# Kernel optimization log

Hardware: AMD Instinct MI355X
Metric: run time of the kernel (lower is better)

## Reference

```python
import jax, jax.numpy as jnp
import numpy as np

N = 100000
E = 1200000


def _gcn_norm(edge_index, num_nodes):
    # Add self-loops and compute symmetric normalization (PyG GCNConv default).
    row = jnp.concatenate([edge_index[0], jnp.arange(num_nodes, dtype=edge_index.dtype)])
    col = jnp.concatenate([edge_index[1], jnp.arange(num_nodes, dtype=edge_index.dtype)])
    deg = jax.ops.segment_sum(jnp.ones_like(col, dtype=jnp.float32), col, num_segments=num_nodes)
    dinv = jnp.where(deg > 0, jax.lax.rsqrt(jnp.maximum(deg, 1.0)), 0.0)
    norm = dinv[row] * dinv[col]  # [E+N]
    return row, col, norm


def _gcn_conv(x, W, b, row, col, norm, num_nodes):
    h = x @ W                      # [N, out] dense transform first (fewer bytes to gather)
    msg = h[row] * norm[:, None]   # gather + edge-wise scale
    out = jax.ops.segment_sum(msg, col, num_segments=num_nodes)  # scatter-add to targets
    return out + b


def setup_inputs() -> dict:
    key = jax.random.key(0)
    k1, k2, k3, k4 = jax.random.split(key, 4)
    x = jax.random.normal(k1, (N, 128), dtype=jnp.float32)
    edge_index = jax.random.randint(k2, (2, E), 0, N, dtype=jnp.int64)
    W1 = jax.random.normal(k3, (128, 256), dtype=jnp.float32) * (1.0 / np.sqrt(128))
    b1 = jnp.zeros((256,), dtype=jnp.float32)
    W2 = jax.random.normal(k4, (256, 40), dtype=jnp.float32) * (1.0 / np.sqrt(256))
    b2 = jnp.zeros((40,), dtype=jnp.float32)
    return {"x": x, "edge_index": edge_index, "W1": W1, "b1": b1, "W2": W2, "b2": b2}


def reference(x, edge_index, W1, b1, W2, b2):
    row, col, norm = _gcn_norm(edge_index, N)
    h = _gcn_conv(x, W1, b1, row, col, norm, N)
    h = jax.nn.relu(h)
    # dropout omitted: eval mode (training=False) is identity
    return _gcn_conv(h, W2, b2, row, col, norm, N)
```

## Files before the change

### kernel.cpp

```cpp
#include <hip/hip_runtime.h>
#include <hip/hip_bf16.h>

#define NN 100000
#define EE 1200000
#define F1 128
#define F2 256
#define F3 40
#define MROWS 64
#define NBUK ((NN + 255) / 256)
#define NBLK 256
#define CHUNK ((EE + NBLK - 1) / NBLK)
#define DCAP 4096
#define XB ((NN * 64 + 255) / 256)

typedef __bf16 bf16x8 __attribute__((ext_vector_type(8)));
typedef float  f32x4  __attribute__((ext_vector_type(4)));

__device__ __forceinline__ unsigned short f2bf(float f) {
    unsigned u = __float_as_uint(f);
    return (unsigned short)((u + 0x7fffu + ((u >> 16) & 1u)) >> 16);
}
__device__ __forceinline__ float bflo(unsigned v) { return __uint_as_float(v << 16); }
__device__ __forceinline__ float bfhi(unsigned v) { return __uint_as_float(v & 0xffff0000u); }

__global__ __launch_bounds__(256) void k_hist(const int* __restrict__ col,
                                              int* __restrict__ hist) {
    __shared__ int lh[NBUK];
    for (int i = threadIdx.x; i < NBUK; i += 256) lh[i] = 0;
    __syncthreads();
    int e0 = blockIdx.x * CHUNK;
    int e1 = min(e0 + CHUNK, EE);
    for (int e = e0 + threadIdx.x; e < e1; e += 256) {
        int c = col[e];
        if ((unsigned)c < (unsigned)NN) atomicAdd(&lh[c >> 8], 1);
    }
    __syncthreads();
    for (int i = threadIdx.x; i < NBUK; i += 256) hist[i * NBLK + blockIdx.x] = lh[i];
}

__global__ __launch_bounds__(256) void k_scanbin(int* __restrict__ hist,
                                                 int* __restrict__ bintot) {
    __shared__ int s[NBLK];
    int b = blockIdx.x;
    int v = hist[b * NBLK + threadIdx.x];
    s[threadIdx.x] = v;
    __syncthreads();
    int acc = v;
    for (int d = 1; d < NBLK; d <<= 1) {
        int add = (threadIdx.x >= d) ? s[threadIdx.x - d] : 0;
        __syncthreads();
        acc += add;
        s[threadIdx.x] = acc;
        __syncthreads();
    }
    hist[b * NBLK + threadIdx.x] = acc - v;
    if (threadIdx.x == NBLK - 1) bintot[b] = acc;
}

__global__ __launch_bounds__(512) void k_scanbase(const int* __restrict__ bintot,
                                                  int* __restrict__ binbase) {
    __shared__ int s[512];
    int v = (threadIdx.x < NBUK) ? bintot[threadIdx.x] : 0;
    s[threadIdx.x] = v;
    __syncthreads();
    int acc = v;
    for (int d = 1; d < 512; d <<= 1) {
        int add = (threadIdx.x >= d) ? s[threadIdx.x - d] : 0;
        __syncthreads();
        acc += add;
        s[threadIdx.x] = acc;
        __syncthreads();
    }
    if (threadIdx.x < NBUK) binbase[threadIdx.x] = acc - v;
    if (threadIdx.x == NBUK - 1) binbase[NBUK] = acc;
}

__global__ __launch_bounds__(256) void k_scat(const int* __restrict__ row,
                                              const int* __restrict__ col,
                                              const int* __restrict__ hist,
                                              const int* __restrict__ binbase,
                                              unsigned* __restrict__ rec) {
    __shared__ int lcur[NBUK];
    for (int i = threadIdx.x; i < NBUK; i += 256)
        lcur[i] = binbase[i] + hist[i * NBLK + blockIdx.x];
    __syncthreads();
    int e0 = blockIdx.x * CHUNK;
    int e1 = min(e0 + CHUNK, EE);
    for (int e = e0 + threadIdx.x; e < e1; e += 256) {
        int r = row[e], c = col[e];
        if ((unsigned)c < (unsigned)NN) {
            int pos = atomicAdd(&lcur[c >> 8], 1);
            rec[pos] = ((unsigned)r & 0xFFFFFFu) | ((unsigned)(c & 255) << 24);
        }
    }
}

__global__ __launch_bounds__(256) void k_csr(const int* __restrict__ binbase,
                                             const unsigned* __restrict__ rec,
                                             int* __restrict__ eidx,
                                             int* __restrict__ cnt,
                                             int* __restrict__ cursor,
                                             float* __restrict__ dinv) {
    __shared__ int lcnt[256];
    __shared__ int s[256];
    __shared__ int lcur[256];
    __shared__ int lde[DCAP];
    const int b = blockIdx.x;
    const int tid = threadIdx.x;
    lcnt[tid] = 0;
    __syncthreads();
    const int base = binbase[b];
    const int nb = min(binbase[b + 1] - base, DCAP);
    for (int j = tid; j < nb; j += 256) atomicAdd(&lcnt[rec[base + j] >> 24], 1);
    __syncthreads();
    int cv = lcnt[tid];
    s[tid] = cv;
    __syncthreads();
    int acc = cv;
    for (int d = 1; d < 256; d <<= 1) {
        int add = (tid >= d) ? s[tid - d] : 0;
        __syncthreads();
        acc += add;
        s[tid] = acc;
        __syncthreads();
    }
    int excl = acc - cv;
    lcur[tid] = excl;
    const int node = (b << 8) + tid;
    if (node < NN) {
        cnt[node] = cv;
        cursor[node] = base + excl + cv;
        dinv[node] = rsqrtf((float)(cv + 1));
    }
    __syncthreads();
    for (int j = tid; j < nb; j += 256) {
        unsigned v = rec[base + j];
        int pos = atomicAdd(&lcur[v >> 24], 1);
        lde[pos] = (int)(v & 0xFFFFFFu);
    }
    __syncthreads();
    for (int j = tid; j < nb; j += 256) eidx[base + j] = lde[j];
}

__global__ void k_prep(const float2* __restrict__ x, const float* __restrict__ dinv,
                       unsigned* __restrict__ xh,
                       const float* __restrict__ W1, const float* __restrict__ W2,
                       __hip_bfloat16* __restrict__ W1p, __hip_bfloat16* __restrict__ W2p) {
    if (blockIdx.x < XB) {
        int idx = blockIdx.x * 256 + threadIdx.x;
        if (idx < NN * 64) {
            float d = dinv[idx >> 6];
            float2 v = x[idx];
            xh[idx] = (unsigned)f2bf(v.x * d) | ((unsigned)f2bf(v.y * d) << 16);
        }
    } else {
        int idx = (blockIdx.x - XB) * 256 + threadIdx.x;
        if (idx < F1 * F2) {
            int k = idx / F2, col = idx - (idx / F2) * F2;
            int k8 = k >> 3, j = k & 7;
            W1p[((size_t)(k8 * F2 + col) << 3) + j] = __float2bfloat16(W1[(size_t)k * F2 + col]);
        } else if (idx < F1 * F2 + F2 * 48) {
            int i2 = idx - F1 * F2;
            int k = i2 / 48, col = i2 - (i2 / 48) * 48;
            int k8 = k >> 3, j = k & 7;
            float v = (col < F3) ? W2[(size_t)k * F3 + col] : 0.0f;
            W2p[((size_t)(k8 * 48 + col) << 3) + j] = __float2bfloat16(v);
        }
    }
}

__global__ __launch_bounds__(256) void k_agg1(const int* __restrict__ cursor,
                                              const int* __restrict__ cnt,
                                              const int* __restrict__ eidx,
                                              const float* __restrict__ dinv,
                                              const unsigned* __restrict__ xh,
                                              unsigned* __restrict__ agg) {
    int node = blockIdx.x * 4 + (threadIdx.x >> 6);
    int lane = threadIdx.x & 63;
    if (node >= NN) return;
    unsigned vs = xh[((size_t)node << 6) + lane];
    float a0 = bflo(vs), a1 = bfhi(vs);
    int n = cnt[node];
    int s = cursor[node] - n;
    int k = 0;
    for (; k + 7 < n; k += 8) {
        int r0 = eidx[s + k + 0], r1 = eidx[s + k + 1];
        int r2 = eidx[s + k + 2], r3 = eidx[s + k + 3];
        int r4 = eidx[s + k + 4], r5 = eidx[s + k + 5];
        int r6 = eidx[s + k + 6], r7 = eidx[s + k + 7];
        unsigned v0 = xh[((size_t)r0 << 6) + lane];
        unsigned v1 = xh[((size_t)r1 << 6) + lane];
        unsigned v2 = xh[((size_t)r2 << 6) + lane];
        unsigned v3 = xh[((size_t)r3 << 6) + lane];
        unsigned v4 = xh[((size_t)r4 << 6) + lane];
        unsigned v5 = xh[((size_t)r5 << 6) + lane];
        unsigned v6 = xh[((size_t)r6 << 6) + lane];
        unsigned v7 = xh[((size_t)r7 << 6) + lane];
        a0 += bflo(v0); a1 += bfhi(v0);
        a0 += bflo(v1); a1 += bfhi(v1);
        a0 += bflo(v2); a1 += bfhi(v2);
        a0 += bflo(v3); a1 += bfhi(v3);
        a0 += bflo(v4); a1 += bfhi(v4);
        a0 += bflo(v5); a1 += bfhi(v5);
        a0 += bflo(v6); a1 += bfhi(v6);
        a0 += bflo(v7); a1 += bfhi(v7);
    }
    for (; k + 3 < n; k += 4) {
        int r0 = eidx[s + k + 0], r1 = eidx[s + k + 1];
        int r2 = eidx[s + k + 2], r3 = eidx[s + k + 3];
        unsigned v0 = xh[((size_t)r0 << 6) + lane];
        unsigned v1 = xh[((size_t)r1 << 6) + lane];
        unsigned v2 = xh[((size_t)r2 << 6) + lane];
        unsigned v3 = xh[((size_t)r3 << 6) + lane];
        a0 += bflo(v0); a1 += bfhi(v0);
        a0 += bflo(v1); a1 += bfhi(v1);
        a0 += bflo(v2); a1 += bfhi(v2);
        a0 += bflo(v3); a1 += bfhi(v3);
    }
    for (; k < n; ++k) {
        unsigned v0 = xh[((size_t)eidx[s + k] << 6) + lane];
        a0 += bflo(v0); a1 += bfhi(v0);
    }
    float d = dinv[node];
    agg[((size_t)node << 6) + lane] = (unsigned)f2bf(a0 * d) | ((unsigned)f2bf(a1 * d) << 16);
}

__global__ __launch_bounds__(256) void k_gemm_mfma(
    const __hip_bfloat16* __restrict__ agg, const __hip_bfloat16* __restrict__ W1p,
    const float* __restrict__ b1, const __hip_bfloat16* __restrict__ W2p,
    const float* __restrict__ dinv, unsigned short* __restrict__ tg) {
    __shared__ __hip_bfloat16 h_s[MROWS][F2 + 8];
    const int i0   = blockIdx.x * MROWS;
    const int wave = threadIdx.x >> 6;
    const int lane = threadIdx.x & 63;
    const int m = lane & 15, q = lane >> 4;
    const int rowA = i0 + wave * 16 + m;

    f32x4 acc[16];
#pragma unroll
    for (int c = 0; c < 16; ++c) acc[c] = (f32x4){0.f, 0.f, 0.f, 0.f};

#pragma unroll
    for (int s = 0; s < 4; ++s) {
        bf16x8 a;
#pragma unroll
        for (int j = 0; j < 8; ++j) a[j] = (__bf16)0.0f;
        if (rowA < NN) a = *(const bf16x8*)(agg + (size_t)rowA * F1 + s * 32 + q * 8);
        const __hip_bfloat16* bp = W1p + ((size_t)(4 * s + q) * F2) * 8;
#pragma unroll
        for (int c = 0; c < 16; ++c) {
            bf16x8 b = *(const bf16x8*)(bp + ((size_t)(c * 16 + m) << 3));
            acc[c] = __builtin_amdgcn_mfma_f32_16x16x32_bf16(a, b, acc[c], 0, 0, 0);
        }
    }

#pragma unroll
    for (int c = 0; c < 16; ++c) {
        int col = c * 16 + m;
        float bj = b1[col];
#pragma unroll
        for (int r = 0; r < 4; ++r) {
            int lr = wave * 16 + q * 4 + r;
            h_s[lr][col] = __float2bfloat16(fmaxf(acc[c][r] + bj, 0.0f));
        }
    }
    __syncthreads();

    f32x4 acc2[3];
#pragma unroll
    for (int c = 0; c < 3; ++c) acc2[c] = (f32x4){0.f, 0.f, 0.f, 0.f};

#pragma unroll
    for (int s = 0; s < 8; ++s) {
        bf16x8 a = *(const bf16x8*)(&h_s[wave * 16 + m][s * 32 + q * 8]);
        const __hip_bfloat16* bp = W2p + ((size_t)(4 * s + q) * 48) * 8;
#pragma unroll
        for (int c = 0; c < 3; ++c) {
            bf16x8 b = *(const bf16x8*)(bp + ((size_t)(c * 16 + m) << 3));
            acc2[c] = __builtin_amdgcn_mfma_f32_16x16x32_bf16(a, b, acc2[c], 0, 0, 0);
        }
    }

#pragma unroll
    for (int c = 0; c < 3; ++c) {
        int col = c * 16 + m;
        if (col < F3) {
#pragma unroll
            for (int r = 0; r < 4; ++r) {
                int grow = i0 + wave * 16 + q * 4 + r;
                if (grow < NN)
                    tg[((size_t)grow << 6) + col] = f2bf(acc2[c][r] * dinv[grow]);
            }
        }
    }
}

__global__ __launch_bounds__(256) void k_agg2(const int* __restrict__ cursor,
                                              const int* __restrict__ cnt,
                                              const int* __restrict__ eidx,
                                              const float* __restrict__ dinv,
                                              const unsigned short* __restrict__ tg,
                                              const float* __restrict__ b2,
                                              float* __restrict__ out) {
    int node = blockIdx.x * 4 + (threadIdx.x >> 6);
    int lane = threadIdx.x & 63;
    if (node >= NN || lane >= F3) return;
    float a = __uint_as_float((unsigned)tg[((size_t)node << 6) + lane] << 16);
    int n = cnt[node];
    int s = cursor[node] - n;
    int k = 0;
    for (; k + 7 < n; k += 8) {
        int r0 = eidx[s + k + 0], r1 = eidx[s + k + 1];
        int r2 = eidx[s + k + 2], r3 = eidx[s + k + 3];
        int r4 = eidx[s + k + 4], r5 = eidx[s + k + 5];
        int r6 = eidx[s + k + 6], r7 = eidx[s + k + 7];
        unsigned short w0 = tg[((size_t)r0 << 6) + lane];
        unsigned short w1 = tg[((size_t)r1 << 6) + lane];
        unsigned short w2 = tg[((size_t)r2 << 6) + lane];
        unsigned short w3 = tg[((size_t)r3 << 6) + lane];
        unsigned short w4 = tg[((size_t)r4 << 6) + lane];
        unsigned short w5 = tg[((size_t)r5 << 6) + lane];
        unsigned short w6 = tg[((size_t)r6 << 6) + lane];
        unsigned short w7 = tg[((size_t)r7 << 6) + lane];
        a += __uint_as_float((unsigned)w0 << 16);
        a += __uint_as_float((unsigned)w1 << 16);
        a += __uint_as_float((unsigned)w2 << 16);
        a += __uint_as_float((unsigned)w3 << 16);
        a += __uint_as_float((unsigned)w4 << 16);
        a += __uint_as_float((unsigned)w5 << 16);
        a += __uint_as_float((unsigned)w6 << 16);
        a += __uint_as_float((unsigned)w7 << 16);
    }
    for (; k + 3 < n; k += 4) {
        int r0 = eidx[s + k + 0], r1 = eidx[s + k + 1];
        int r2 = eidx[s + k + 2], r3 = eidx[s + k + 3];
        unsigned short w0 = tg[((size_t)r0 << 6) + lane];
        unsigned short w1 = tg[((size_t)r1 << 6) + lane];
        unsigned short w2 = tg[((size_t)r2 << 6) + lane];
        unsigned short w3 = tg[((size_t)r3 << 6) + lane];
        a += __uint_as_float((unsigned)w0 << 16);
        a += __uint_as_float((unsigned)w1 << 16);
        a += __uint_as_float((unsigned)w2 << 16);
        a += __uint_as_float((unsigned)w3 << 16);
    }
    for (; k < n; ++k)
        a += __uint_as_float((unsigned)tg[((size_t)eidx[s + k] << 6) + lane] << 16);
    out[(size_t)node * F3 + lane] = dinv[node] * a + b2[lane];
}

extern "C" void kernel_launch(void* const* d_in, const int* in_sizes, int n_in,
                              void* d_out, int out_size, void* d_ws, size_t ws_size,
                              hipStream_t stream) {
    const float* x  = (const float*)d_in[0];
    const int*   ei = (const int*)d_in[1];
    const float* W1 = (const float*)d_in[2];
    const float* b1 = (const float*)d_in[3];
    const float* W2 = (const float*)d_in[4];
    const float* b2 = (const float*)d_in[5];
    float* out = (float*)d_out;

    const int* row = ei;
    const int* col = ei + EE;

    int* cnt     = (int*)d_ws;
    int* cursor  = cnt + NN;
    float* dinv  = (float*)(cursor + NN);
    int* hist    = (int*)(dinv + NN);
    int* bintot  = hist + NBUK * NBLK;
    int* binbase = bintot + NBUK;
    int* eidx    = binbase + (NBUK + 1) + 7;
    unsigned* xh  = (unsigned*)(eidx + EE);
    unsigned* agg = xh + (size_t)NN * 64;
    unsigned* rec = agg;
    unsigned short* tg = (unsigned short*)xh;
    __hip_bfloat16* W1p = (__hip_bfloat16*)(agg + (size_t)NN * 64);
    __hip_bfloat16* W2p = W1p + (size_t)F1 * F2;

    k_hist    <<<NBLK, 256, 0, stream>>>(col, hist);
    k_scanbin <<<NBUK, NBLK, 0, stream>>>(hist, bintot);
    k_scanbase<<<1, 512, 0, stream>>>(bintot, binbase);
    k_scat    <<<NBLK, 256, 0, stream>>>(row, col, hist, binbase, rec);
    k_csr     <<<NBUK, 256, 0, stream>>>(binbase, rec, eidx, cnt, cursor, dinv);

    k_prep<<<XB + (F1 * F2 + F2 * 48 + 255) / 256, 256, 0, stream>>>(
        (const float2*)x, dinv, xh, W1, W2, W1p, W2p);

    k_agg1<<<(NN + 3) / 4, 256, 0, stream>>>(cursor, cnt, eidx, dinv, xh, agg);
    k_gemm_mfma<<<(NN + MROWS - 1) / MROWS, 256, 0, stream>>>(
        (const __hip_bfloat16*)agg, W1p, b1, W2p, dinv, tg);
    k_agg2<<<(NN + 3) / 4, 256, 0, stream>>>(cursor, cnt, eidx, dinv, tg, b2, out);
}
```

Before: 301.5 us.

## Split layer-1 aggregation into two feature halves with edge-parallel 16-byte gathers

Layer-1 aggregation now runs as two passes, each covering half of the 128 bf16 features (64 per pass). Within a wave, 8 lane groups each take different edges and load 16 bytes per lane, and the partial sums are combined with xor shuffles. Halving the gathered slice per pass shrinks the working set of xh that must stay cache-resident, and the wider loads cut instruction count. The prep kernel also vectorises to float4 loads, and the eidx workspace offset is shifted, apparently to keep the xh pointer 16-byte aligned. The cost is an extra kernel launch, the edge indices are read twice, and there is shuffle-reduction overhead.

```diff
diff --git a/kernel.cpp b/kernel.cpp
--- a/kernel.cpp
+++ b/kernel.cpp
@@ -11,7 +11,7 @@
 #define NBLK 256
 #define CHUNK ((EE + NBLK - 1) / NBLK)
 #define DCAP 4096
-#define XB ((NN * 64 + 255) / 256)
+#define XB2 ((NN * 32 + 255) / 256)
 
 typedef __bf16 bf16x8 __attribute__((ext_vector_type(8)));
 typedef float  f32x4  __attribute__((ext_vector_type(4)));
@@ -142,19 +142,20 @@
     for (int j = tid; j < nb; j += 256) eidx[base + j] = lde[j];
 }
 
-__global__ void k_prep(const float2* __restrict__ x, const float* __restrict__ dinv,
-                       unsigned* __restrict__ xh,
+__global__ void k_prep(const float4* __restrict__ x, const float* __restrict__ dinv,
+                       uint2* __restrict__ xh,
                        const float* __restrict__ W1, const float* __restrict__ W2,
                        __hip_bfloat16* __restrict__ W1p, __hip_bfloat16* __restrict__ W2p) {
-    if (blockIdx.x < XB) {
+    if (blockIdx.x < XB2) {
         int idx = blockIdx.x * 256 + threadIdx.x;
-        if (idx < NN * 64) {
-            float d = dinv[idx >> 6];
-            float2 v = x[idx];
-            xh[idx] = (unsigned)f2bf(v.x * d) | ((unsigned)f2bf(v.y * d) << 16);
-        }
+        float d = dinv[idx >> 5];
+        float4 v = x[idx];
+        uint2 o;
+        o.x = (unsigned)f2bf(v.x * d) | ((unsigned)f2bf(v.y * d) << 16);
+        o.y = (unsigned)f2bf(v.z * d) | ((unsigned)f2bf(v.w * d) << 16);
+        xh[idx] = o;
     } else {
-        int idx = (blockIdx.x - XB) * 256 + threadIdx.x;
+        int idx = (blockIdx.x - XB2) * 256 + threadIdx.x;
         if (idx < F1 * F2) {
             int k = idx / F2, col = idx - (idx / F2) * F2;
             int k8 = k >> 3, j = k & 7;
@@ -174,55 +175,55 @@
                                               const int* __restrict__ eidx,
                                               const float* __restrict__ dinv,
                                               const unsigned* __restrict__ xh,
-                                              unsigned* __restrict__ agg) {
+                                              unsigned* __restrict__ agg,
+                                              int p) {
     int node = blockIdx.x * 4 + (threadIdx.x >> 6);
-    int lane = threadIdx.x & 63;
     if (node >= NN) return;
-    unsigned vs = xh[((size_t)node << 6) + lane];
-    float a0 = bflo(vs), a1 = bfhi(vs);
-    int n = cnt[node];
-    int s = cursor[node] - n;
-    int k = 0;
-    for (; k + 7 < n; k += 8) {
-        int r0 = eidx[s + k + 0], r1 = eidx[s + k + 1];
-        int r2 = eidx[s + k + 2], r3 = eidx[s + k + 3];
-        int r4 = eidx[s + k + 4], r5 = eidx[s + k + 5];
-        int r6 = eidx[s + k + 6], r7 = eidx[s + k + 7];
-        unsigned v0 = xh[((size_t)r0 << 6) + lane];
-        unsigned v1 = xh[((size_t)r1 << 6) + lane];
-        unsigned v2 = xh[((size_t)r2 << 6) + lane];
-        unsigned v3 = xh[((size_t)r3 << 6) + lane];
-        unsigned v4 = xh[((size_t)r4 << 6) + lane];
-        unsigned v5 = xh[((size_t)r5 << 6) + lane];
-        unsigned v6 = xh[((size_t)r6 << 6) + lane];
-        unsigned v7 = xh[((size_t)r7 << 6) + lane];
-        a0 += bflo(v0); a1 += bfhi(v0);
-        a0 += bflo(v1); a1 += bfhi(v1);
-        a0 += bflo(v2); a1 += bfhi(v2);
-        a0 += bflo(v3); a1 += bfhi(v3);
-        a0 += bflo(v4); a1 += bfhi(v4);
-        a0 += bflo(v5); a1 += bfhi(v5);
-        a0 += bflo(v6); a1 += bfhi(v6);
-        a0 += bflo(v7); a1 += bfhi(v7);
-    }
-    for (; k + 3 < n; k += 4) {
-        int r0 = eidx[s + k + 0], r1 = eidx[s + k + 1];
-        int r2 = eidx[s + k + 2], r3 = eidx[s + k + 3];
-        unsigned v0 = xh[((size_t)r0 << 6) + lane];
-        unsigned v1 = xh[((size_t)r1 << 6) + lane];
-        unsigned v2 = xh[((size_t)r2 << 6) + lane];
-        unsigned v3 = xh[((size_t)r3 << 6) + lane];
-        a0 += bflo(v0); a1 += bfhi(v0);
-        a0 += bflo(v1); a1 += bfhi(v1);
-        a0 += bflo(v2); a1 += bfhi(v2);
-        a0 += bflo(v3); a1 += bfhi(v3);
-    }
-    for (; k < n; ++k) {
-        unsigned v0 = xh[((size_t)eidx[s + k] << 6) + lane];
-        a0 += bflo(v0); a1 += bfhi(v0);
-    }
-    float d = dinv[node];
-    agg[((size_t)node << 6) + lane] = (unsigned)f2bf(a0 * d) | ((unsigned)f2bf(a1 * d) << 16);
+    const int lane = threadIdx.x & 63;
+    const int g = lane >> 3, t = lane & 7;
+    const uint4* __restrict__ xb = (const uint4*)(xh + p * 32) + t;
+
+    float a0 = 0.f, a1 = 0.f, a2 = 0.f, a3 = 0.f, a4 = 0.f, a5 = 0.f, a6 = 0.f, a7 = 0.f;
+    if (g == 0) {
+        uint4 v = xb[(size_t)node << 4];
+        a0 = bflo(v.x); a1 = bfhi(v.x); a2 = bflo(v.y); a3 = bfhi(v.y);
+        a4 = bflo(v.z); a5 = bfhi(v.z); a6 = bflo(v.w); a7 = bfhi(v.w);
+    }
+    const int n = cnt[node];
+    const int s = cursor[node] - n;
+    int k = g;
+    for (; k + 8 < n; k += 16) {
+        int r0 = eidx[s + k];
+        int r1 = eidx[s + k + 8];
+        uint4 v0 = xb[(size_t)r0 << 4];
+        uint4 v1 = xb[(size_t)r1 << 4];
+        a0 += bflo(v0.x); a1 += bfhi(v0.x); a2 += bflo(v0.y); a3 += bfhi(v0.y);
+        a4 += bflo(v0.z); a5 += bfhi(v0.z); a6 += bflo(v0.w); a7 += bfhi(v0.w);
+        a0 += bflo(v1.x); a1 += bfhi(v1.x); a2 += bflo(v1.y); a3 += bfhi(v1.y);
+        a4 += bflo(v1.z); a5 += bfhi(v1.z); a6 += bflo(v1.w); a7 += bfhi(v1.w);
+    }
+    if (k < n) {
+        int r0 = eidx[s + k];
+        uint4 v0 = xb[(size_t)r0 << 4];
+        a0 += bflo(v0.x); a1 += bfhi(v0.x); a2 += bflo(v0.y); a3 += bfhi(v0.y);
+        a4 += bflo(v0.z); a5 += bfhi(v0.z); a6 += bflo(v0.w); a7 += bfhi(v0.w);
+    }
+#pragma unroll
+    for (int off = 8; off < 64; off <<= 1) {
+        a0 += __shfl_xor(a0, off); a1 += __shfl_xor(a1, off);
+        a2 += __shfl_xor(a2, off); a3 += __shfl_xor(a3, off);
+        a4 += __shfl_xor(a4, off); a5 += __shfl_xor(a5, off);
+        a6 += __shfl_xor(a6, off); a7 += __shfl_xor(a7, off);
+    }
+    if (g == 0) {
+        float d = dinv[node];
+        uint4 o;
+        o.x = (unsigned)f2bf(a0 * d) | ((unsigned)f2bf(a1 * d) << 16);
+        o.y = (unsigned)f2bf(a2 * d) | ((unsigned)f2bf(a3 * d) << 16);
+        o.z = (unsigned)f2bf(a4 * d) | ((unsigned)f2bf(a5 * d) << 16);
+        o.w = (unsigned)f2bf(a6 * d) | ((unsigned)f2bf(a7 * d) << 16);
+        *(uint4*)(agg + ((size_t)node << 6) + p * 32 + (t << 2)) = o;
+    }
 }
 
 __global__ __launch_bounds__(256) void k_gemm_mfma(
@@ -368,7 +369,7 @@
     int* hist    = (int*)(dinv + NN);
     int* bintot  = hist + NBUK * NBLK;
     int* binbase = bintot + NBUK;
-    int* eidx    = binbase + (NBUK + 1) + 7;
+    int* eidx    = binbase + (NBUK + 1) + 9;
     unsigned* xh  = (unsigned*)(eidx + EE);
     unsigned* agg = xh + (size_t)NN * 64;
     unsigned* rec = agg;
@@ -382,10 +383,11 @@
     k_scat    <<<NBLK, 256, 0, stream>>>(row, col, hist, binbase, rec);
     k_csr     <<<NBUK, 256, 0, stream>>>(binbase, rec, eidx, cnt, cursor, dinv);
 
-    k_prep<<<XB + (F1 * F2 + F2 * 48 + 255) / 256, 256, 0, stream>>>(
-        (const float2*)x, dinv, xh, W1, W2, W1p, W2p);
-
-    k_agg1<<<(NN + 3) / 4, 256, 0, stream>>>(cursor, cnt, eidx, dinv, xh, agg);
+    k_prep<<<XB2 + (F1 * F2 + F2 * 48 + 255) / 256, 256, 0, stream>>>(
+        (const float4*)x, dinv, (uint2*)xh, W1, W2, W1p, W2p);
+
+    k_agg1<<<(NN + 3) / 4, 256, 0, stream>>>(cursor, cnt, eidx, dinv, xh, agg, 0);
+    k_agg1<<<(NN + 3) / 4, 256, 0, stream>>>(cursor, cnt, eidx, dinv, xh, agg, 1);
     k_gemm_mfma<<<(NN + MROWS - 1) / MROWS, 256, 0, stream>>>(
         (const __hip_bfloat16*)agg, W1p, b1, W2p, dinv, tg);
     k_agg2<<<(NN + 3) / 4, 256, 0, stream>>>(cursor, cnt, eidx, dinv, tg, b2, out);
```

Result: slower. 332.9 us (+10.4%).
